# Kernel tuning notes

Hardware: AMD Instinct MI355X
Metric: run time of the kernel (lower is better)

## Reference

```python
import jax, jax.numpy as jnp
import numpy as np

WINDOW = 128
LOOK_BACKWARD = 1
LOOK_FORWARD = 0
DIM_HEAD = 64
ROPE_BASE = 10000.0


def look_around(x, backward=LOOK_BACKWARD, forward=LOOK_FORWARD, pad_value=-1):
    # x: [b, w, n, ...] -> pad window axis, gather shifted windows, concat along n axis
    w = x.shape[1]
    pads = [(0, 0)] * x.ndim
    pads[1] = (backward, forward)
    padded = jnp.pad(x, pads, constant_values=pad_value)
    return jnp.concatenate([padded[:, i:i + w] for i in range(backward + forward + 1)], axis=2)


def _rotate_half(x):
    x1, x2 = jnp.split(x, 2, axis=-1)
    return jnp.concatenate([-x2, x1], axis=-1)


def apply_rotary(bq, bk):
    # sinusoidal embeddings computed over the look-around key length j; queries use the last n positions
    j = bk.shape[2]
    n = bq.shape[2]
    inv_freq = 1.0 / (ROPE_BASE ** (jnp.arange(0, DIM_HEAD, 2, dtype=jnp.float32) / DIM_HEAD))
    t = jnp.arange(j, dtype=jnp.float32)
    freqs = t[:, None] * inv_freq[None, :]          # [j, d/2]
    freqs = jnp.concatenate([freqs, freqs], axis=-1)  # [j, d]
    q_freqs = freqs[-n:]
    bq = bq * jnp.cos(q_freqs) + _rotate_half(bq) * jnp.sin(q_freqs)
    bk = bk * jnp.cos(freqs) + _rotate_half(bk) * jnp.sin(freqs)
    return bq, bk


def setup_inputs() -> dict:
    key = jax.random.key(0)
    kq, kk, kv = jax.random.split(key, 3)
    shape = (4, 8, 4096, 64)
    return {
        'q': jax.random.normal(kq, shape, dtype=jnp.float32),
        'k': jax.random.normal(kk, shape, dtype=jnp.float32),
        'v': jax.random.normal(kv, shape, dtype=jnp.float32),
    }


def reference(q, k, v):
    B, H, N, D = q.shape
    b = B * H
    q_ = q.reshape(b, N, D)
    k_ = k.reshape(b, N, D)
    v_ = v.reshape(b, N, D)
    w = N // WINDOW
    scale = D ** -0.5

    seq = jnp.arange(N)
    b_t = seq.reshape(1, w, WINDOW)                           # [1, w, n]

    bq = q_.reshape(b, w, WINDOW, D) * scale
    bk = look_around(k_.reshape(b, w, WINDOW, D), pad_value=-1.0)  # [b, w, j, d]
    bv = look_around(v_.reshape(b, w, WINDOW, D), pad_value=-1.0)

    bq, bk = apply_rotary(bq, bk)

    bq_t = b_t[..., :, None]                                  # [1, w, n, 1]
    bq_k = look_around(b_t, pad_value=-1)[..., None, :]        # [1, w, 1, j]
    pad_mask = bq_k == -1
    causal_mask = bq_t < bq_k

    sim = jnp.einsum('bwie,bwje->bwij', bq, bk)                # [b, w, n, j]
    mask_value = -jnp.finfo(sim.dtype).max
    sim = jnp.where(causal_mask | pad_mask, mask_value, sim)

    attn = jax.nn.softmax(sim, axis=-1)
    out = jnp.einsum('bwij,bwje->bwie', attn, bv)
    return out.reshape(B, H, N, D)
```

## Files before the change

### kernel.cpp

```cpp
#include <hip/hip_runtime.h>
#include <float.h>

typedef __attribute__((ext_vector_type(8))) _Float16 f16x8;
typedef __attribute__((ext_vector_type(4))) _Float16 f16x4;
typedef __attribute__((ext_vector_type(4))) float f32x4;

#define WIN 128
#define SEQ 4096
#define DH 64
#define KSTR 72
#define VSTR 260
#define PC 40
#define VOFF 36864
#define POFF (VOFF + DH * VSTR * 2)
#define L2B_OVER 0.41524101186092156f

__launch_bounds__(512, 4)
__global__ void lattn_kernel(const float* __restrict__ q,
                             const float* __restrict__ k,
                             const float* __restrict__ v,
                             float* __restrict__ out) {
  __shared__ __align__(16) char smem[POFF + 8 * 16 * PC * 2];
  _Float16* ksm = (_Float16*)smem;
  _Float16* vsm = (_Float16*)(smem + VOFF);
  _Float16* psm = (_Float16*)(smem + POFF);

  const int bid  = blockIdx.x;
  const int lbid = (bid & 7) * 128 + (bid >> 3);
  const int bh   = lbid >> 5;
  const int win  = lbid & 31;
  const int tid  = threadIdx.x;
  const int wv   = tid >> 6;
  const int lane = tid & 63;
  const int c    = lane & 15;
  const int g    = lane >> 4;

  const long kbase = (long)win * WIN - WIN;
  const float* kb = k + (size_t)bh * SEQ * DH;
  const float* vb = v + (size_t)bh * SEQ * DH;

  #pragma unroll
  for (int it = 0; it < 4; ++it) {
    int hi  = it * 8 + wv;
    int row = c + 16 * (hi >> 1);
    int p   = g + 4 * (hi & 1);
    long grow = kbase + row; grow = grow < 0 ? 0 : grow;
    const float4* src = (const float4*)(kb + grow * DH);
    float4 lo  = src[p];
    float4 hi4 = src[p + 8];
    float pos = (float)row;
    f16x4 rl, rh;
    #pragma unroll
    for (int j = 0; j < 4; ++j) {
      float sn, cs;
      __sincosf(pos * exp2f(-(float)(4 * p + j) * L2B_OVER), &sn, &cs);
      float x = ((const float*)&lo)[j];
      float y = ((const float*)&hi4)[j];
      rl[j] = (_Float16)(x * cs - y * sn);
      rh[j] = (_Float16)(y * cs + x * sn);
    }
    *(f16x4*)(&ksm[row * KSTR + 4 * p])      = rl;
    *(f16x4*)(&ksm[row * KSTR + 4 * p + 32]) = rh;
  }

  #pragma unroll
  for (int it = 0; it < 2; ++it) {
    int kq = g + 4 * (it * 8 + wv);
    int dq = c;
    float4 r[4];
    #pragma unroll
    for (int i = 0; i < 4; ++i) {
      long grow = kbase + 4 * kq + i; grow = grow < 0 ? 0 : grow;
      r[i] = *(const float4*)(vb + grow * DH + 4 * dq);
    }
    #pragma unroll
    for (int j = 0; j < 4; ++j) {
      f16x4 w;
      #pragma unroll
      for (int i = 0; i < 4; ++i) w[i] = (_Float16)(((const float*)&r[i])[j]);
      *(f16x4*)(&vsm[(4 * dq + j) * VSTR + 4 * kq]) = w;
    }
  }

  const int qrow = 16 * wv + c;
  const float* qp = q + ((size_t)bh * SEQ + (size_t)win * WIN + qrow) * DH;
  const float4 x0 = *(const float4*)(qp + 8 * g);
  const float4 x1 = *(const float4*)(qp + 8 * g + 4);
  const float4 y0 = *(const float4*)(qp + 8 * g + 32);
  const float4 y1 = *(const float4*)(qp + 8 * g + 36);
  f16x8 qf0, qf1;
  {
    float pos = (float)(128 + qrow);
    #pragma unroll
    for (int j = 0; j < 4; ++j) {
      float sn, cs;
      __sincosf(pos * exp2f(-(float)(8 * g + j) * L2B_OVER), &sn, &cs);
      float xa = ((const float*)&x0)[j], ya = ((const float*)&y0)[j];
      qf0[j]     = (_Float16)((xa * cs - ya * sn) * 0.125f);
      qf1[j]     = (_Float16)((ya * cs + xa * sn) * 0.125f);
      __sincosf(pos * exp2f(-(float)(8 * g + 4 + j) * L2B_OVER), &sn, &cs);
      float xb = ((const float*)&x1)[j], yb = ((const float*)&y1)[j];
      qf0[4 + j] = (_Float16)((xb * cs - yb * sn) * 0.125f);
      qf1[4 + j] = (_Float16)((yb * cs + xb * sn) * 0.125f);
    }
  }

  __syncthreads();

  f32x4 acc[16];
  #pragma unroll
  for (int mt = 0; mt < 16; ++mt) acc[mt] = (f32x4){0.f, 0.f, 0.f, 0.f};

  #pragma unroll
  for (int mt = 0; mt < 16; ++mt) {
    f16x8 kf0 = *(const f16x8*)(&ksm[(16 * mt + c) * KSTR + 8 * g]);
    f16x8 kf1 = *(const f16x8*)(&ksm[(16 * mt + c) * KSTR + 32 + 8 * g]);
    acc[mt] = __builtin_amdgcn_mfma_f32_16x16x32_f16(kf0, qf0, acc[mt], 0, 0, 0);
    acc[mt] = __builtin_amdgcn_mfma_f32_16x16x32_f16(kf1, qf1, acc[mt], 0, 0, 0);
  }

  const int qi   = qrow;
  const int kmin = (win == 0) ? 128 : 0;
  float m = -FLT_MAX;
  #pragma unroll
  for (int mt = 0; mt < 16; ++mt) {
    #pragma unroll
    for (int r = 0; r < 4; ++r) {
      int j = 16 * mt + 4 * g + r;
      bool ok = (j <= qi + 128) && (j >= kmin);
      float s = ok ? acc[mt][r] : -FLT_MAX;
      acc[mt][r] = s;
      m = fmaxf(m, s);
    }
  }
  m = fmaxf(m, __shfl_xor(m, 16));
  m = fmaxf(m, __shfl_xor(m, 32));

  float sm = 0.f;
  #pragma unroll
  for (int mt = 0; mt < 16; ++mt) {
    #pragma unroll
    for (int r = 0; r < 4; ++r) {
      float p = __expf(acc[mt][r] - m);
      acc[mt][r] = p;
      sm += p;
    }
  }
  sm += __shfl_xor(sm, 16);
  sm += __shfl_xor(sm, 32);
  const float rinv = 1.0f / sm;

  f32x4 oacc[4];
  #pragma unroll
  for (int nt = 0; nt < 4; ++nt) oacc[nt] = (f32x4){0.f, 0.f, 0.f, 0.f};

  _Float16* pw = psm + wv * 16 * PC;

  #pragma unroll
  for (int ks = 0; ks < 8; ++ks) {
    if (ks) {
      asm volatile("s_waitcnt lgkmcnt(0)" ::: "memory");
      __builtin_amdgcn_sched_barrier(0);
    }
    #pragma unroll
    for (int t = 0; t < 2; ++t) {
      int mt = 2 * ks + t;
      f16x4 pv4;
      #pragma unroll
      for (int r = 0; r < 4; ++r) pv4[r] = (_Float16)(acc[mt][r] * rinv);
      *(f16x4*)(&pw[c * PC + 16 * t + 4 * g]) = pv4;
    }
    asm volatile("s_waitcnt lgkmcnt(0)" ::: "memory");
    __builtin_amdgcn_sched_barrier(0);

    f16x8 pf = *(const f16x8*)(&pw[c * PC + 8 * g]);
    #pragma unroll
    for (int nt = 0; nt < 4; ++nt) {
      f16x8 vf = *(const f16x8*)(&vsm[(16 * nt + c) * VSTR + 32 * ks + 8 * g]);
      oacc[nt] = __builtin_amdgcn_mfma_f32_16x16x32_f16(pf, vf, oacc[nt], 0, 0, 0);
    }
  }

  float* ob = out + ((size_t)bh * SEQ + (size_t)win * WIN + 16 * wv) * DH;
  #pragma unroll
  for (int nt = 0; nt < 4; ++nt) {
    #pragma unroll
    for (int r = 0; r < 4; ++r) {
      ob[(4 * g + r) * DH + 16 * nt + c] = oacc[nt][r];
    }
  }
}

extern "C" void kernel_launch(void* const* d_in, const int* in_sizes, int n_in,
                              void* d_out, int out_size, void* d_ws, size_t ws_size,
                              hipStream_t stream) {
  const float* q = (const float*)d_in[0];
  const float* k = (const float*)d_in[1];
  const float* v = (const float*)d_in[2];
  float* out = (float*)d_out;
  dim3 grid(32 * 32);
  lattn_kernel<<<grid, 512, 0, stream>>>(q, k, v, out);
}
```

Before: 52.65 us.

## Hoist K/V/Q global loads ahead of conversion, swap PV MFMA operands for float4 stores

```diff
diff --git a/kernel.cpp b/kernel.cpp
--- a/kernel.cpp
+++ b/kernel.cpp
@@ -39,6 +39,8 @@
   const float* kb = k + (size_t)bh * SEQ * DH;
   const float* vb = v + (size_t)bh * SEQ * DH;
 
+
+  float4 klo[4], khi[4];
   #pragma unroll
   for (int it = 0; it < 4; ++it) {
     int hi  = it * 8 + wv;
@@ -46,39 +48,18 @@
     int p   = g + 4 * (hi & 1);
     long grow = kbase + row; grow = grow < 0 ? 0 : grow;
     const float4* src = (const float4*)(kb + grow * DH);
-    float4 lo  = src[p];
-    float4 hi4 = src[p + 8];
-    float pos = (float)row;
-    f16x4 rl, rh;
-    #pragma unroll
-    for (int j = 0; j < 4; ++j) {
-      float sn, cs;
-      __sincosf(pos * exp2f(-(float)(4 * p + j) * L2B_OVER), &sn, &cs);
-      float x = ((const float*)&lo)[j];
-      float y = ((const float*)&hi4)[j];
-      rl[j] = (_Float16)(x * cs - y * sn);
-      rh[j] = (_Float16)(y * cs + x * sn);
-    }
-    *(f16x4*)(&ksm[row * KSTR + 4 * p])      = rl;
-    *(f16x4*)(&ksm[row * KSTR + 4 * p + 32]) = rh;
-  }
-
+    klo[it] = src[p];
+    khi[it] = src[p + 8];
+  }
+
+  float4 vr[2][4];
   #pragma unroll
   for (int it = 0; it < 2; ++it) {
     int kq = g + 4 * (it * 8 + wv);
-    int dq = c;
-    float4 r[4];
     #pragma unroll
     for (int i = 0; i < 4; ++i) {
       long grow = kbase + 4 * kq + i; grow = grow < 0 ? 0 : grow;
-      r[i] = *(const float4*)(vb + grow * DH + 4 * dq);
-    }
-    #pragma unroll
-    for (int j = 0; j < 4; ++j) {
-      f16x4 w;
-      #pragma unroll
-      for (int i = 0; i < 4; ++i) w[i] = (_Float16)(((const float*)&r[i])[j]);
-      *(f16x4*)(&vsm[(4 * dq + j) * VSTR + 4 * kq]) = w;
+      vr[it][i] = *(const float4*)(vb + grow * DH + 4 * c);
     }
   }
 
@@ -88,6 +69,39 @@
   const float4 x1 = *(const float4*)(qp + 8 * g + 4);
   const float4 y0 = *(const float4*)(qp + 8 * g + 32);
   const float4 y1 = *(const float4*)(qp + 8 * g + 36);
+
+  #pragma unroll
+  for (int it = 0; it < 4; ++it) {
+    int hi  = it * 8 + wv;
+    int row = c + 16 * (hi >> 1);
+    int p   = g + 4 * (hi & 1);
+    float pos = (float)row;
+    f16x4 rl, rh;
+    #pragma unroll
+    for (int j = 0; j < 4; ++j) {
+      float sn, cs;
+      __sincosf(pos * exp2f(-(float)(4 * p + j) * L2B_OVER), &sn, &cs);
+      float x = ((const float*)&klo[it])[j];
+      float y = ((const float*)&khi[it])[j];
+      rl[j] = (_Float16)(x * cs - y * sn);
+      rh[j] = (_Float16)(y * cs + x * sn);
+    }
+    *(f16x4*)(&ksm[row * KSTR + 4 * p])      = rl;
+    *(f16x4*)(&ksm[row * KSTR + 4 * p + 32]) = rh;
+  }
+
+  #pragma unroll
+  for (int it = 0; it < 2; ++it) {
+    int kq = g + 4 * (it * 8 + wv);
+    #pragma unroll
+    for (int j = 0; j < 4; ++j) {
+      f16x4 w;
+      #pragma unroll
+      for (int i = 0; i < 4; ++i) w[i] = (_Float16)(((const float*)&vr[it][i])[j]);
+      *(f16x4*)(&vsm[(4 * c + j) * VSTR + 4 * kq]) = w;
+    }
+  }
+
   f16x8 qf0, qf1;
   {
     float pos = (float)(128 + qrow);
@@ -158,10 +172,6 @@
 
   #pragma unroll
   for (int ks = 0; ks < 8; ++ks) {
-    if (ks) {
-      asm volatile("s_waitcnt lgkmcnt(0)" ::: "memory");
-      __builtin_amdgcn_sched_barrier(0);
-    }
     #pragma unroll
     for (int t = 0; t < 2; ++t) {
       int mt = 2 * ks + t;
@@ -170,24 +180,19 @@
       for (int r = 0; r < 4; ++r) pv4[r] = (_Float16)(acc[mt][r] * rinv);
       *(f16x4*)(&pw[c * PC + 16 * t + 4 * g]) = pv4;
     }
-    asm volatile("s_waitcnt lgkmcnt(0)" ::: "memory");
-    __builtin_amdgcn_sched_barrier(0);
-
     f16x8 pf = *(const f16x8*)(&pw[c * PC + 8 * g]);
     #pragma unroll
     for (int nt = 0; nt < 4; ++nt) {
       f16x8 vf = *(const f16x8*)(&vsm[(16 * nt + c) * VSTR + 32 * ks + 8 * g]);
-      oacc[nt] = __builtin_amdgcn_mfma_f32_16x16x32_f16(pf, vf, oacc[nt], 0, 0, 0);
-    }
-  }
-
-  float* ob = out + ((size_t)bh * SEQ + (size_t)win * WIN + 16 * wv) * DH;
+      oacc[nt] = __builtin_amdgcn_mfma_f32_16x16x32_f16(vf, pf, oacc[nt], 0, 0, 0);
+    }
+  }
+
+  float* ob = out + ((size_t)bh * SEQ + (size_t)win * WIN + qrow) * DH;
   #pragma unroll
   for (int nt = 0; nt < 4; ++nt) {
-    #pragma unroll
-    for (int r = 0; r < 4; ++r) {
-      ob[(4 * g + r) * DH + 16 * nt + c] = oacc[nt][r];
-    }
+    float4 o4 = {oacc[nt][0], oacc[nt][1], oacc[nt][2], oacc[nt][3]};
+    *(float4*)(ob + 16 * nt + 4 * g) = o4;
   }
 }
 
```

After: 53.10 us. About the same (+0.9%).
